# Kernel tuning notes

Measured on AMD Instinct MI355X. Metric: run time of the kernel, lower is better.

## Reference

```python
import jax, jax.numpy as jnp
import numpy as np

B, T, D = 2, 2048, 1024
N, H = 16, 64  # num_heads, head_dim
LOG2E = 1.442695041
NEG_INF = -1.0e9


def setup_inputs() -> dict:
    key = jax.random.key(0)
    ks = jax.random.split(key, 6)
    return {
        "input_tensor": jax.random.normal(ks[0], (B, T, D), dtype=jnp.float32),
        "attention_mask": jax.random.randint(ks[1], (B, 1, T, T), 0, 2, dtype=jnp.int32),
        "wq": jax.random.normal(ks[2], (D, N, H), dtype=jnp.float32),
        "bq": jnp.zeros((N, H), dtype=jnp.float32),
        "wk": jax.random.normal(ks[3], (D, N, H), dtype=jnp.float32),
        "bk": jnp.zeros((N, H), dtype=jnp.float32),
        "wv": jax.random.normal(ks[4], (D, N, H), dtype=jnp.float32),
        "bv": jnp.zeros((N, H), dtype=jnp.float32),
        "wo": jax.random.normal(ks[5], (D, N, H), dtype=jnp.float32),
        "bo": jnp.zeros((D,), dtype=jnp.float32),
        "per_dim_scale": jnp.zeros((H,), dtype=jnp.float32),
    }


def reference(input_tensor, attention_mask, wq, bq, wk, bk, wv, bv, wo, bo, per_dim_scale):
    # QKV projections: [B,T,D] x [D,N,H] -> [B,T,N,H]
    q = jnp.einsum('btd,dnh->btnh', input_tensor, wq) + bq
    k = jnp.einsum('btd,dnh->btnh', input_tensor, wk) + bk
    v = jnp.einsum('btd,dnh->btnh', input_tensor, wv) + bv
    # per-dim query scaling: (log2(e)/sqrt(H)) * softplus(per_dim_scale)
    scale = (LOG2E / jnp.sqrt(jnp.asarray(H, q.dtype))) * jax.nn.softplus(per_dim_scale)
    q = q * scale
    # scores: [B,N,T,S]
    scores = jnp.einsum('btnh,bsnh->bnts', q, k)
    scores = jnp.where(attention_mask == 0, jnp.asarray(NEG_INF, scores.dtype), scores)
    weights = jax.nn.softmax(scores, axis=-1)
    # AV: [B,N,T,S] x [B,S,N,H] -> [B,T,N,H]
    attn_out = jnp.einsum('bnts,bsnh->btnh', weights, v)
    # output projection: [B,T,N,H] x [D,N,H] -> [B,T,D]
    return jnp.einsum('btnh,dnh->btd', attn_out, wo) + bo
```

## Files before the change

kernel.cpp:

```cpp
#include <hip/hip_runtime.h>
#include <math.h>

typedef __bf16 bf16;
typedef __attribute__((ext_vector_type(8))) __bf16 bf16x8;
typedef __attribute__((ext_vector_type(4))) __bf16 bf16x4;
typedef __attribute__((ext_vector_type(4))) float f32x4;

#define BB 2
#define TT 2048
#define DD 1024
#define NHD 16
#define HD 64
#define MM (BB*TT)
#define LOG2E_F 1.442695041f
#define NEGINF_F (-1.0e9f)

__device__ __forceinline__ void gld16(const bf16* g, bf16* l)
{
    __builtin_amdgcn_global_load_lds(
        (const __attribute__((address_space(1))) unsigned int*)g,
        (__attribute__((address_space(3))) unsigned int*)l, 16, 0, 0);
}

__global__ __launch_bounds__(256)
void prep_all(const float* __restrict__ X, const int* __restrict__ m,
              const float* __restrict__ wq, const float* __restrict__ wk,
              const float* __restrict__ wv, const float* __restrict__ wo,
              bf16* __restrict__ Xh, bf16* __restrict__ Xl,
              bf16* __restrict__ qkh, bf16* __restrict__ qkl,
              bf16* __restrict__ vh, bf16* __restrict__ ob,
              unsigned char* __restrict__ bits)
{
    __shared__ float tile[32][33];
    const int bid = blockIdx.x;
    const int t   = threadIdx.x;

    if (bid < 4096) {
        int i = bid * 256 + t;
        float4 v = ((const float4*)X)[i];
        float f[4] = {v.x, v.y, v.z, v.w};
        bf16x4 h, l;
        #pragma unroll
        for (int j = 0; j < 4; ++j) {
            bf16 hh = (bf16)f[j];
            h[j] = hh;
            l[j] = (bf16)(f[j] - (float)hh);
        }
        *(bf16x4*)(Xh + (size_t)i * 4) = h;
        *(bf16x4*)(Xl + (size_t)i * 4) = l;
        return;
    }
    if (bid < 8192) {
        const int idx = bid - 4096;
        const int z   = idx >> 10;
        const int bx  = (idx & 31) << 5;
        const int by  = ((idx >> 5) & 31) << 5;
        const int r   = t >> 3;
        const int c4  = (t & 7) << 2;
        if (z == 3) {
            float4 v = *(const float4*)(wo + (size_t)(by + r) * 1024 + bx + c4);
            bf16x4 o = { (bf16)v.x, (bf16)v.y, (bf16)v.z, (bf16)v.w };
            *(bf16x4*)(ob + (size_t)(by + r) * 1024 + bx + c4) = o;
            return;
        }
        const float* src = (z == 0) ? wq : ((z == 1) ? wk : wv);
        bf16* oh = (z == 0) ? qkh : ((z == 1) ? qkh + 1048576 : vh);
        bf16* ol = (z == 0) ? qkl : ((z == 1) ? qkl + 1048576 : nullptr);
        float4 v = *(const float4*)(src + (size_t)(by + r) * 1024 + bx + c4);
        tile[r][c4+0] = v.x; tile[r][c4+1] = v.y;
        tile[r][c4+2] = v.z; tile[r][c4+3] = v.w;
        __syncthreads();
        bf16x4 hv, lv;
        #pragma unroll
        for (int j = 0; j < 4; ++j) {
            float f = tile[c4 + j][r];
            bf16 h = (bf16)f;
            hv[j] = h;
            lv[j] = (bf16)(f - (float)h);
        }
        *(bf16x4*)(oh + (size_t)(bx + r) * 1024 + by + c4) = hv;
        if (ol)
            *(bf16x4*)(ol + (size_t)(bx + r) * 1024 + by + c4) = lv;
        return;
    }
    {
        int i = (bid - 8192) * 256 + t;
        const int4* mp = (const int4*)m + (size_t)i * 2;
        int4 a  = mp[0];
        int4 b4 = mp[1];
        unsigned v = (a.x  != 0)       | ((a.y  != 0) << 1)
                   | ((a.z  != 0) << 2) | ((a.w  != 0) << 3)
                   | ((b4.x != 0) << 4) | ((b4.y != 0) << 5)
                   | ((b4.z != 0) << 6) | ((b4.w != 0) << 7);
        bits[i] = (unsigned char)v;
    }
}

__global__ __launch_bounds__(256)
void gemm_proj(const bf16* __restrict__ Xh, const bf16* __restrict__ Xl,
               const bf16* __restrict__ Wh, const bf16* __restrict__ Wl,
               const bf16* __restrict__ Wvh,
               const float* __restrict__ bq, const float* __restrict__ bk,
               const float* __restrict__ bv, const float* __restrict__ pds,
               bf16* __restrict__ oQh, bf16* __restrict__ oQl,
               bf16* __restrict__ oKh, bf16* __restrict__ oKl,
               bf16* __restrict__ oVt)
{
    __shared__ bf16 S[4][128 * 32];

    const int bid  = blockIdx.x;
    const int t    = threadIdx.x;
    const int lane = t & 63;
    const int w    = t >> 6;
    const int quad = lane >> 4, l15 = lane & 15;
    const int wm   = (w >> 1) << 6;
    const int wn   = (w & 1)  << 6;

    const int jr0 = ((w * 2 + 0) << 4) + (lane >> 2);
    const int jr1 = ((w * 2 + 1) << 4) + (lane >> 2);
    const int kch = (lane & 3) << 3;
    const int off0 = (w * 2 + 0) * 512;
    const int off1 = (w * 2 + 1) * 512;

    if (bid < 512) {
        const int m0 = (bid >> 4) << 7;
        const int n0 = (bid & 15) << 7;
        bf16* Ah = S[0]; bf16* Al = S[1]; bf16* Bh = S[2]; bf16* Bl = S[3];

        const bf16* pAh0 = Xh + (size_t)(m0 + jr0) * DD + kch;
        const bf16* pAh1 = Xh + (size_t)(m0 + jr1) * DD + kch;
        const bf16* pAl0 = Xl + (size_t)(m0 + jr0) * DD + kch;
        const bf16* pAl1 = Xl + (size_t)(m0 + jr1) * DD + kch;
        const bf16* pBh0 = Wh + (size_t)(n0 + jr0) * DD + kch;
        const bf16* pBh1 = Wh + (size_t)(n0 + jr1) * DD + kch;
        const bf16* pBl0 = Wl + (size_t)(n0 + jr0) * DD + kch;
        const bf16* pBl1 = Wl + (size_t)(n0 + jr1) * DD + kch;

        f32x4 acc[4][4] = {};

        for (int k0 = 0; k0 < DD; k0 += 32) {
            __syncthreads();
            gld16(pAh0 + k0, Ah + off0);  gld16(pAh1 + k0, Ah + off1);
            gld16(pAl0 + k0, Al + off0);  gld16(pAl1 + k0, Al + off1);
            gld16(pBh0 + k0, Bh + off0);  gld16(pBh1 + k0, Bh + off1);
            gld16(pBl0 + k0, Bl + off0);  gld16(pBl1 + k0, Bl + off1);
            __syncthreads();

            bf16x8 ah[4], bh[4];
            #pragma unroll
            for (int mt = 0; mt < 4; ++mt)
                ah[mt] = *(const bf16x8*)(Ah + (wm + (mt << 4) + l15) * 32 + (quad << 3));
            #pragma unroll
            for (int nt = 0; nt < 4; ++nt)
                bh[nt] = *(const bf16x8*)(Bh + (wn + (nt << 4) + l15) * 32 + (quad << 3));
            #pragma unroll
            for (int mt = 0; mt < 4; ++mt)
                #pragma unroll
                for (int nt = 0; nt < 4; ++nt)
                    acc[mt][nt] = __builtin_amdgcn_mfma_f32_16x16x32_bf16(
                        ah[mt], bh[nt], acc[mt][nt], 0, 0, 0);

            bf16x8 bl[4];
            #pragma unroll
            for (int nt = 0; nt < 4; ++nt)
                bl[nt] = *(const bf16x8*)(Bl + (wn + (nt << 4) + l15) * 32 + (quad << 3));
            #pragma unroll
            for (int mt = 0; mt < 4; ++mt)
                #pragma unroll
                for (int nt = 0; nt < 4; ++nt)
                    acc[mt][nt] = __builtin_amdgcn_mfma_f32_16x16x32_bf16(
                        ah[mt], bl[nt], acc[mt][nt], 0, 0, 0);

            bf16x8 al[4];
            #pragma unroll
            for (int mt = 0; mt < 4; ++mt)
                al[mt] = *(const bf16x8*)(Al + (wm + (mt << 4) + l15) * 32 + (quad << 3));
            #pragma unroll
            for (int mt = 0; mt < 4; ++mt)
                #pragma unroll
                for (int nt = 0; nt < 4; ++nt)
                    acc[mt][nt] = __builtin_amdgcn_mfma_f32_16x16x32_bf16(
                        al[mt], bh[nt], acc[mt][nt], 0, 0, 0);
        }

        #pragma unroll
        for (int nt = 0; nt < 4; ++nt) {
            const int col = n0 + wn + (nt << 4) + l15;
            const int isQ = (col < 1024);
            const int nh  = col & 1023;
            const int n   = nh >> 6, h = nh & 63;
            const float bcol = isQ ? bq[nh] : bk[nh];
            float s = 1.f;
            if (isQ) {
                float x  = pds[h];
                float sp = fmaxf(x, 0.f) + log1pf(expf(-fabsf(x)));
                s = (LOG2E_F * LOG2E_F / 8.0f) * sp;
            }
            bf16* dH = isQ ? oQh : oKh;
            bf16* dL = isQ ? oQl : oKl;
            #pragma unroll
            for (int mt = 0; mt < 4; ++mt) {
                #pragma unroll
                for (int reg = 0; reg < 4; ++reg) {
                    const int row = m0 + wm + (mt << 4) + (quad << 2) + reg;
                    const int bi  = row >> 11;
                    const int tt  = row & (TT - 1);
                    float val = (acc[mt][nt][reg] + bcol) * s;
                    const size_t idx = (((size_t)bi * NHD + n) * TT + tt) * HD + h;
                    bf16 hi = (bf16)val;
                    dH[idx] = hi;
                    dL[idx] = (bf16)(val - (float)hi);
                }
            }
        }
    } else {
        const int idx = bid - 512;
        const int m0  = (idx >> 5) << 7;
        const int n0  = (idx & 31) << 7;
        bf16* As = S[0]; bf16* Bs = S[2];

        const bf16* Ap0 = Wvh + (size_t)(m0 + jr0) * DD + kch;
        const bf16* Ap1 = Wvh + (size_t)(m0 + jr1) * DD + kch;
        const bf16* Bp0 = Xh  + (size_t)(n0 + jr0) * DD + kch;
        const bf16* Bp1 = Xh  + (size_t)(n0 + jr1) * DD + kch;

        f32x4 acc[4][4] = {};

        for (int k0 = 0; k0 < DD; k0 += 32) {
            __syncthreads();
            gld16(Ap0 + k0, As + off0);
            gld16(Ap1 + k0, As + off1);
            gld16(Bp0 + k0, Bs + off0);
            gld16(Bp1 + k0, Bs + off1);
            __syncthreads();
            bf16x8 af[4], bfm[4];
            #pragma unroll
            for (int mt = 0; mt < 4; ++mt)
                af[mt] = *(const bf16x8*)(As + (wm + (mt << 4) + l15) * 32 + (quad << 3));
            #pragma unroll
            for (int nt = 0; nt < 4; ++nt)
                bfm[nt] = *(const bf16x8*)(Bs + (wn + (nt << 4) + l15) * 32 + (quad << 3));
            #pragma unroll
            for (int mt = 0; mt < 4; ++mt)
                #pragma unroll
                for (int nt = 0; nt < 4; ++nt)
                    acc[mt][nt] = __builtin_amdgcn_mfma_f32_16x16x32_bf16(
                        af[mt], bfm[nt], acc[mt][nt], 0, 0, 0);
        }

        #pragma unroll
        for (int nt = 0; nt < 4; ++nt) {
            const int col = n0 + wn + (nt << 4) + l15;
            const int bi  = col >> 11;
            const int tt  = col & (TT - 1);
            #pragma unroll
            for (int mt = 0; mt < 4; ++mt) {
                #pragma unroll
                for (int reg = 0; reg < 4; ++reg) {
                    const int row = m0 + wm + (mt << 4) + (quad << 2) + reg;
                    float val = acc[mt][nt][reg] + bv[row];
                    oVt[((size_t)bi * 1024 + row) * TT + tt] = (bf16)val;
                }
            }
        }
    }
}

__global__ __launch_bounds__(256)
void gemm_out(const bf16* __restrict__ A, const bf16* __restrict__ Bt,
              const float* __restrict__ bias, float* __restrict__ oF)
{
    __shared__ bf16 As[128 * 32];
    __shared__ bf16 Bs[64 * 32];

    const int t    = threadIdx.x;
    const int lane = t & 63;
    const int w    = t >> 6;
    const int quad = lane >> 4, l15 = lane & 15;
    const int m0   = blockIdx.y << 7;
    const int n0   = blockIdx.x << 6;
    const int wm   = (w >> 1) << 6;
    const int wn   = (w & 1)  << 5;

    const int jr0 = ((w * 2 + 0) << 4) + (lane >> 2);
    const int jr1 = ((w * 2 + 1) << 4) + (lane >> 2);
    const int jrB = (w << 4) + (lane >> 2);
    const int kch = (lane & 3) << 3;

    bf16* lA0 = As + (w * 2 + 0) * 512;
    bf16* lA1 = As + (w * 2 + 1) * 512;
    bf16* lB  = Bs + w * 512;

    const bf16* Ap0 = A  + (size_t)(m0 + jr0) * DD + kch;
    const bf16* Ap1 = A  + (size_t)(m0 + jr1) * DD + kch;
    const bf16* Bp  = Bt + (size_t)(n0 + jrB) * DD + kch;

    f32x4 acc[4][2] = {};

    for (int k0 = 0; k0 < DD; k0 += 32) {
        __syncthreads();
        gld16(Ap0 + k0, lA0);
        gld16(Ap1 + k0, lA1);
        gld16(Bp + k0, lB);
        __syncthreads();
        bf16x8 af[4], bfm[2];
        #pragma unroll
        for (int mt = 0; mt < 4; ++mt)
            af[mt] = *(const bf16x8*)(As + (wm + (mt << 4) + l15) * 32 + (quad << 3));
        #pragma unroll
        for (int nt = 0; nt < 2; ++nt)
            bfm[nt] = *(const bf16x8*)(Bs + (wn + (nt << 4) + l15) * 32 + (quad << 3));
        #pragma unroll
        for (int mt = 0; mt < 4; ++mt)
            #pragma unroll
            for (int nt = 0; nt < 2; ++nt)
                acc[mt][nt] = __builtin_amdgcn_mfma_f32_16x16x32_bf16(
                    af[mt], bfm[nt], acc[mt][nt], 0, 0, 0);
    }

    #pragma unroll
    for (int nt = 0; nt < 2; ++nt) {
        const int col = n0 + wn + (nt << 4) + l15;
        const float bcol = bias[col];
        #pragma unroll
        for (int mt = 0; mt < 4; ++mt) {
            #pragma unroll
            for (int reg = 0; reg < 4; ++reg) {
                const int row = m0 + wm + (mt << 4) + (quad << 2) + reg;
                oF[(size_t)row * DD + col] = acc[mt][nt][reg] + bcol;
            }
        }
    }
}

__global__ __launch_bounds__(512)
void attn_mfma(const bf16* __restrict__ Qh, const bf16* __restrict__ Ql,
               const bf16* __restrict__ Kh, const bf16* __restrict__ Kl,
               const bf16* __restrict__ Vt,
               const unsigned long long* __restrict__ mb64,
               bf16* __restrict__ AO)
{
    __shared__ bf16 Ksh[64][64];
    __shared__ bf16 Ksl[64][64];
    __shared__ bf16 Vts[64][64];
    __shared__ bf16 Ps[8][16][64];
    __shared__ unsigned long long msk64[128];

    const int t    = threadIdx.x;
    const int lane = t & 63;
    const int w    = t >> 6;
    const int quad = lane >> 4, l15 = lane & 15;
    const int bn   = blockIdx.y;
    const int b    = bn >> 4, n = bn & 15;
    const int q0   = blockIdx.x << 7;

    const bf16* Qbh = Qh + (size_t)bn * TT * HD;
    const bf16* Qbl = Ql + (size_t)bn * TT * HD;
    const bf16* Kbh = Kh + (size_t)bn * TT * HD;
    const bf16* Kbl = Kl + (size_t)bn * TT * HD;
    const bf16* Vtb = Vt + (size_t)bn * HD * TT;

    const int qrow = q0 + (w << 4) + l15;
    bf16x8 qfh[2], qfl[2];
    qfh[0] = *(const bf16x8*)(Qbh + (size_t)qrow * HD + (quad << 3));
    qfh[1] = *(const bf16x8*)(Qbh + (size_t)qrow * HD + 32 + (quad << 3));
    qfl[0] = *(const bf16x8*)(Qbl + (size_t)qrow * HD + (quad << 3));
    qfl[1] = *(const bf16x8*)(Qbl + (size_t)qrow * HD + 32 + (quad << 3));

    f32x4 O[4];
    #pragma unroll
    for (int i = 0; i < 4; ++i) O[i] = (f32x4){0.f,0.f,0.f,0.f};
    float m_i = -INFINITY;
    float l_i = 0.f;

    const int rS = t >> 3;
    const int cG = (t & 7) << 3;
    const int cL = (((t & 7) ^ (rS & 7)) << 3);
    const int sw8 = (l15 & 7) << 3;

    for (int kb = 0; kb < TT; kb += 64) {
        bf16x8 khv = *(const bf16x8*)(Kbh + (size_t)(kb + rS) * HD + cG);
        bf16x8 klv = *(const bf16x8*)(Kbl + (size_t)(kb + rS) * HD + cG);
        bf16x8 vv  = *(const bf16x8*)(Vtb + (size_t)rS * TT + kb + cG);
        unsigned long long mw = 0;
        if (t < 128)
            mw = mb64[((size_t)b * TT + q0 + t) * (TT / 64) + (kb >> 6)];

        __syncthreads();
        *(bf16x8*)&Ksh[rS][cL] = khv;
        *(bf16x8*)&Ksl[rS][cL] = klv;
        *(bf16x8*)&Vts[rS][cL] = vv;
        if (t < 128) msk64[t] = mw;
        __syncthreads();

        f32x4 s_acc[4];
        #pragma unroll
        for (int i = 0; i < 4; ++i) s_acc[i] = (f32x4){0.f,0.f,0.f,0.f};
        __builtin_amdgcn_s_setprio(1);
        #pragma unroll
        for (int k2 = 0; k2 < 2; ++k2) {
            #pragma unroll
            for (int nt = 0; nt < 4; ++nt) {
                bf16x8 bkh = *(const bf16x8*)&Ksh[(nt << 4) + l15][((k2 << 5) + (quad << 3)) ^ sw8];
                bf16x8 bkl = *(const bf16x8*)&Ksl[(nt << 4) + l15][((k2 << 5) + (quad << 3)) ^ sw8];
                s_acc[nt] = __builtin_amdgcn_mfma_f32_16x16x32_bf16(bkh, qfh[k2], s_acc[nt], 0, 0, 0);
                s_acc[nt] = __builtin_amdgcn_mfma_f32_16x16x32_bf16(bkl, qfh[k2], s_acc[nt], 0, 0, 0);
                s_acc[nt] = __builtin_amdgcn_mfma_f32_16x16x32_bf16(bkh, qfl[k2], s_acc[nt], 0, 0, 0);
            }
        }
        __builtin_amdgcn_s_setprio(0);

        const unsigned long long word = msk64[(w << 4) + l15];
        const unsigned w0 = (unsigned)word;
        const unsigned w1 = (unsigned)(word >> 32);
        float sv[16];
        #pragma unroll
        for (int nt = 0; nt < 4; ++nt) {
            const unsigned wrd = (nt & 2) ? w1 : w0;
            #pragma unroll
            for (int reg = 0; reg < 4; ++reg) {
                const int bit = ((nt & 1) << 4) + (quad << 2) + reg;
                sv[nt * 4 + reg] = ((wrd >> bit) & 1u) ? s_acc[nt][reg] : NEGINF_F;
            }
        }
        float a0 = fmaxf(sv[0], sv[1]),  a1 = fmaxf(sv[2], sv[3]);
        float a2 = fmaxf(sv[4], sv[5]),  a3 = fmaxf(sv[6], sv[7]);
        float a4 = fmaxf(sv[8], sv[9]),  a5 = fmaxf(sv[10], sv[11]);
        float a6 = fmaxf(sv[12], sv[13]), a7 = fmaxf(sv[14], sv[15]);
        float b0 = fmaxf(a0, a1), b1 = fmaxf(a2, a3);
        float b2 = fmaxf(a4, a5), b3 = fmaxf(a6, a7);
        float mx = fmaxf(fmaxf(b0, b1), fmaxf(b2, b3));
        mx = fmaxf(mx, __shfl_xor(mx, 16));
        mx = fmaxf(mx, __shfl_xor(mx, 32));

        if (!__all(mx <= m_i + 8.0f)) {
            const float mnew  = fmaxf(m_i, mx);
            const float alpha = exp2f(m_i - mnew);
            l_i *= alpha;
            #pragma unroll
            for (int nt = 0; nt < 4; ++nt) {
                O[nt][0] *= alpha; O[nt][1] *= alpha;
                O[nt][2] *= alpha; O[nt][3] *= alpha;
            }
            m_i = mnew;
        }

        float p[16];
        #pragma unroll
        for (int i = 0; i < 16; ++i) p[i] = exp2f(sv[i] - m_i);
        float s0 = (p[0] + p[1]) + (p[2] + p[3]);
        float s1 = (p[4] + p[5]) + (p[6] + p[7]);
        float s2 = (p[8] + p[9]) + (p[10] + p[11]);
        float s3 = (p[12] + p[13]) + (p[14] + p[15]);
        float sum = (s0 + s1) + (s2 + s3);
        sum += __shfl_xor(sum, 16);
        sum += __shfl_xor(sum, 32);
        l_i += sum;

        #pragma unroll
        for (int nt = 0; nt < 4; ++nt) {
            bf16x4 pv = { (bf16)p[nt * 4 + 0], (bf16)p[nt * 4 + 1],
                          (bf16)p[nt * 4 + 2], (bf16)p[nt * 4 + 3] };
            *(bf16x4*)&Ps[w][l15][((nt << 4) + (quad << 2)) ^ sw8] = pv;
        }

        __builtin_amdgcn_s_setprio(1);
        #pragma unroll
        for (int s2i = 0; s2i < 2; ++s2i) {
            bf16x8 ap = *(const bf16x8*)&Ps[w][l15][((s2i << 5) + (quad << 3)) ^ sw8];
            #pragma unroll
            for (int nt = 0; nt < 4; ++nt) {
                bf16x8 bv = *(const bf16x8*)&Vts[(nt << 4) + l15][((s2i << 5) + (quad << 3)) ^ sw8];
                O[nt] = __builtin_amdgcn_mfma_f32_16x16x32_bf16(bv, ap, O[nt], 0, 0, 0);
            }
        }
        __builtin_amdgcn_s_setprio(0);
    }

    {
        const float inv = 1.0f / l_i;
        const size_t base = ((size_t)b * TT + qrow) * (NHD * HD) + (size_t)n * HD;
        #pragma unroll
        for (int nt = 0; nt < 4; ++nt) {
            bf16x4 o = { (bf16)(O[nt][0] * inv), (bf16)(O[nt][1] * inv),
                         (bf16)(O[nt][2] * inv), (bf16)(O[nt][3] * inv) };
            *(bf16x4*)(AO + base + (nt << 4) + (quad << 2)) = o;
        }
    }
}

extern "C" void kernel_launch(void* const* d_in, const int* in_sizes, int n_in,
                              void* d_out, int out_size, void* d_ws, size_t ws_size,
                              hipStream_t stream)
{
    const float* X   = (const float*)d_in[0];
    const int*   msk = (const int*)d_in[1];
    const float* wq  = (const float*)d_in[2];
    const float* bq  = (const float*)d_in[3];
    const float* wk  = (const float*)d_in[4];
    const float* bk  = (const float*)d_in[5];
    const float* wv  = (const float*)d_in[6];
    const float* bv  = (const float*)d_in[7];
    const float* wo  = (const float*)d_in[8];
    const float* bo  = (const float*)d_in[9];
    const float* pds = (const float*)d_in[10];
    float* out = (float*)d_out;

    bf16* ws   = (bf16*)d_ws;
    bf16* Xh   = ws;
    bf16* Xl   = ws + 4194304;
    bf16* WQKh = ws + 8388608;
    bf16* WQKl = ws + 10485760;
    bf16* Wvh  = ws + 12582912;
    bf16* Wob  = ws + 13631488;
    bf16* Qhb  = ws + 14680064;
    bf16* Qlb  = ws + 18874368;
    bf16* Khb  = ws + 23068672;
    bf16* Klb  = ws + 27262976;
    unsigned char* mbits = (unsigned char*)(ws + 31457280);
    bf16* Vtb  = ws + 32505856;
    bf16* AOb  = Xh;

    dim3 blk(256);

    prep_all<<<12288, blk, 0, stream>>>(X, msk, wq, wk, wv, wo,
                                        Xh, Xl, WQKh, WQKl, Wvh, Wob, mbits);

    gemm_proj<<<768, blk, 0, stream>>>(
        Xh, Xl, WQKh, WQKl, Wvh, bq, bk, bv, pds,
        Qhb, Qlb, Khb, Klb, Vtb);

    dim3 ga(TT / 128, BB * NHD);
    attn_mfma<<<ga, dim3(512), 0, stream>>>(
        Qhb, Qlb, Khb, Klb, Vtb, (const unsigned long long*)mbits, AOb);

    gemm_out<<<dim3(16, 32), blk, 0, stream>>>(AOb, Wob, bo, out);
}
```

Baseline: 312.9 us.

## Split attention KV range across two warp groups with in-block softmax merge

```diff
diff --git a/kernel.cpp b/kernel.cpp
--- a/kernel.cpp
+++ b/kernel.cpp
@@ -333,26 +333,26 @@
     }
 }
 
-__global__ __launch_bounds__(512)
+__global__ __launch_bounds__(512, 6)
 void attn_mfma(const bf16* __restrict__ Qh, const bf16* __restrict__ Ql,
                const bf16* __restrict__ Kh, const bf16* __restrict__ Kl,
                const bf16* __restrict__ Vt,
                const unsigned long long* __restrict__ mb64,
                bf16* __restrict__ AO)
 {
-    __shared__ bf16 Ksh[64][64];
-    __shared__ bf16 Ksl[64][64];
-    __shared__ bf16 Vts[64][64];
-    __shared__ bf16 Ps[8][16][64];
-    __shared__ unsigned long long msk64[128];
+    __shared__ bf16 KH[2][64 * 64];
+    __shared__ bf16 KL[2][64 * 64];
+    __shared__ bf16 PS[8][16 * 64];
+    __shared__ unsigned long long MSK[2][64];
 
     const int t    = threadIdx.x;
     const int lane = t & 63;
     const int w    = t >> 6;
+    const int g    = w >> 2;
     const int quad = lane >> 4, l15 = lane & 15;
     const int bn   = blockIdx.y;
     const int b    = bn >> 4, n = bn & 15;
-    const int q0   = blockIdx.x << 7;
+    const int q0   = blockIdx.x << 6;
 
     const bf16* Qbh = Qh + (size_t)bn * TT * HD;
     const bf16* Qbl = Ql + (size_t)bn * TT * HD;
@@ -360,7 +360,7 @@
     const bf16* Kbl = Kl + (size_t)bn * TT * HD;
     const bf16* Vtb = Vt + (size_t)bn * HD * TT;
 
-    const int qrow = q0 + (w << 4) + l15;
+    const int qrow = q0 + ((w & 3) << 4) + l15;
     bf16x8 qfh[2], qfl[2];
     qfh[0] = *(const bf16x8*)(Qbh + (size_t)qrow * HD + (quad << 3));
     qfh[1] = *(const bf16x8*)(Qbh + (size_t)qrow * HD + 32 + (quad << 3));
@@ -373,24 +373,37 @@
     float m_i = -INFINITY;
     float l_i = 0.f;
 
-    const int rS = t >> 3;
-    const int cG = (t & 7) << 3;
-    const int cL = (((t & 7) ^ (rS & 7)) << 3);
+    const int tg  = t & 255;
+    const int rS  = tg >> 2;
+    const int cp  = tg & 3;
+    const int cG0 = (cp * 2    ) << 3;
+    const int cG1 = (cp * 2 + 1) << 3;
+    const int cL0 = (((cp * 2    ) ^ (rS & 7))) << 3;
+    const int cL1 = (((cp * 2 + 1) ^ (rS & 7))) << 3;
     const int sw8 = (l15 & 7) << 3;
 
-    for (int kb = 0; kb < TT; kb += 64) {
-        bf16x8 khv = *(const bf16x8*)(Kbh + (size_t)(kb + rS) * HD + cG);
-        bf16x8 klv = *(const bf16x8*)(Kbl + (size_t)(kb + rS) * HD + cG);
-        bf16x8 vv  = *(const bf16x8*)(Vtb + (size_t)rS * TT + kb + cG);
+    for (int it = 0; it < 16; ++it) {
+        const int kb = (g << 10) + (it << 6);
+        const bf16* kr = Kbh + (size_t)(kb + rS) * HD;
+        const bf16* lr = Kbl + (size_t)(kb + rS) * HD;
+        const bf16* vr = Vtb + (size_t)rS * TT + kb;
+        bf16x8 kh0 = *(const bf16x8*)(kr + cG0);
+        bf16x8 kh1 = *(const bf16x8*)(kr + cG1);
+        bf16x8 kl0 = *(const bf16x8*)(lr + cG0);
+        bf16x8 kl1 = *(const bf16x8*)(lr + cG1);
+        bf16x8 v0  = *(const bf16x8*)(vr + cG0);
+        bf16x8 v1  = *(const bf16x8*)(vr + cG1);
         unsigned long long mw = 0;
         if (t < 128)
-            mw = mb64[((size_t)b * TT + q0 + t) * (TT / 64) + (kb >> 6)];
-
-        __syncthreads();
-        *(bf16x8*)&Ksh[rS][cL] = khv;
-        *(bf16x8*)&Ksl[rS][cL] = klv;
-        *(bf16x8*)&Vts[rS][cL] = vv;
-        if (t < 128) msk64[t] = mw;
+            mw = mb64[((size_t)b * TT + q0 + (t & 63)) * (TT / 64)
+                      + ((t >> 6) << 4) + it];
+
+        __syncthreads();
+        *(bf16x8*)&KH[g][rS * 64 + cL0] = kh0;
+        *(bf16x8*)&KH[g][rS * 64 + cL1] = kh1;
+        *(bf16x8*)&KL[g][rS * 64 + cL0] = kl0;
+        *(bf16x8*)&KL[g][rS * 64 + cL1] = kl1;
+        if (t < 128) MSK[t >> 6][t & 63] = mw;
         __syncthreads();
 
         f32x4 s_acc[4];
@@ -401,8 +414,10 @@
         for (int k2 = 0; k2 < 2; ++k2) {
             #pragma unroll
             for (int nt = 0; nt < 4; ++nt) {
-                bf16x8 bkh = *(const bf16x8*)&Ksh[(nt << 4) + l15][((k2 << 5) + (quad << 3)) ^ sw8];
-                bf16x8 bkl = *(const bf16x8*)&Ksl[(nt << 4) + l15][((k2 << 5) + (quad << 3)) ^ sw8];
+                const int ro = ((nt << 4) + l15) * 64;
+                const int co = ((k2 << 5) + (quad << 3)) ^ sw8;
+                bf16x8 bkh = *(const bf16x8*)&KH[g][ro + co];
+                bf16x8 bkl = *(const bf16x8*)&KL[g][ro + co];
                 s_acc[nt] = __builtin_amdgcn_mfma_f32_16x16x32_bf16(bkh, qfh[k2], s_acc[nt], 0, 0, 0);
                 s_acc[nt] = __builtin_amdgcn_mfma_f32_16x16x32_bf16(bkl, qfh[k2], s_acc[nt], 0, 0, 0);
                 s_acc[nt] = __builtin_amdgcn_mfma_f32_16x16x32_bf16(bkh, qfl[k2], s_acc[nt], 0, 0, 0);
@@ -410,7 +425,7 @@
         }
         __builtin_amdgcn_s_setprio(0);
 
-        const unsigned long long word = msk64[(w << 4) + l15];
+        const unsigned long long word = MSK[g][((w & 3) << 4) + l15];
         const unsigned w0 = (unsigned)word;
         const unsigned w1 = (unsigned)(word >> 32);
         float sv[16];
@@ -461,30 +476,65 @@
         for (int nt = 0; nt < 4; ++nt) {
             bf16x4 pv = { (bf16)p[nt * 4 + 0], (bf16)p[nt * 4 + 1],
                           (bf16)p[nt * 4 + 2], (bf16)p[nt * 4 + 3] };
-            *(bf16x4*)&Ps[w][l15][((nt << 4) + (quad << 2)) ^ sw8] = pv;
-        }
+            *(bf16x4*)&PS[w][l15 * 64 + (((nt << 4) + (quad << 2)) ^ sw8)] = pv;
+        }
+
+        __syncthreads();
+        *(bf16x8*)&KL[g][rS * 64 + cL0] = v0;
+        *(bf16x8*)&KL[g][rS * 64 + cL1] = v1;
+        __syncthreads();
 
         __builtin_amdgcn_s_setprio(1);
         #pragma unroll
         for (int s2i = 0; s2i < 2; ++s2i) {
-            bf16x8 ap = *(const bf16x8*)&Ps[w][l15][((s2i << 5) + (quad << 3)) ^ sw8];
+            bf16x8 ap = *(const bf16x8*)&PS[w][l15 * 64 + (((s2i << 5) + (quad << 3)) ^ sw8)];
             #pragma unroll
             for (int nt = 0; nt < 4; ++nt) {
-                bf16x8 bv = *(const bf16x8*)&Vts[(nt << 4) + l15][((s2i << 5) + (quad << 3)) ^ sw8];
+                bf16x8 bv = *(const bf16x8*)&KL[g][((nt << 4) + l15) * 64
+                                                   + (((s2i << 5) + (quad << 3)) ^ sw8)];
                 O[nt] = __builtin_amdgcn_mfma_f32_16x16x32_bf16(bv, ap, O[nt], 0, 0, 0);
             }
         }
         __builtin_amdgcn_s_setprio(0);
     }
 
-    {
-        const float inv = 1.0f / l_i;
-        const size_t base = ((size_t)b * TT + qrow) * (NHD * HD) + (size_t)n * HD;
+    float* OMp = (float*)&KH[0][0];
+    float* MLp = (float*)&KL[0][0];
+    __syncthreads();
+    if (w >= 4) {
+        const int base = (w - 4) << 10;
+        #pragma unroll
+        for (int nt = 0; nt < 4; ++nt)
+            #pragma unroll
+            for (int reg = 0; reg < 4; ++reg) {
+                const int h = (nt << 4) + (quad << 2) + reg;
+                OMp[base + h * 16 + l15] = O[nt][reg];
+            }
+        if (quad == 0) {
+            MLp[((w - 4) << 5) + (l15 << 1)    ] = m_i;
+            MLp[((w - 4) << 5) + (l15 << 1) + 1] = l_i;
+        }
+    }
+    __syncthreads();
+    if (w < 4) {
+        const float m1v = MLp[(w << 5) + (l15 << 1)];
+        const float l1v = MLp[(w << 5) + (l15 << 1) + 1];
+        const float mm  = fmaxf(m_i, m1v);
+        const float f0  = exp2f(m_i - mm);
+        const float f1  = exp2f(m1v - mm);
+        const float inv = 1.0f / (l_i * f0 + l1v * f1);
+        const int   ob  = w << 10;
+        const size_t basew = ((size_t)b * TT + qrow) * (NHD * HD) + (size_t)n * HD;
         #pragma unroll
         for (int nt = 0; nt < 4; ++nt) {
-            bf16x4 o = { (bf16)(O[nt][0] * inv), (bf16)(O[nt][1] * inv),
-                         (bf16)(O[nt][2] * inv), (bf16)(O[nt][3] * inv) };
-            *(bf16x4*)(AO + base + (nt << 4) + (quad << 2)) = o;
+            bf16x4 o;
+            #pragma unroll
+            for (int reg = 0; reg < 4; ++reg) {
+                const int h = (nt << 4) + (quad << 2) + reg;
+                const float o1 = OMp[ob + h * 16 + l15];
+                o[reg] = (bf16)((O[nt][reg] * f0 + o1 * f1) * inv);
+            }
+            *(bf16x4*)(AO + basew + (nt << 4) + (quad << 2)) = o;
         }
     }
 }
@@ -530,7 +580,7 @@
         Xh, Xl, WQKh, WQKl, Wvh, bq, bk, bv, pds,
         Qhb, Qlb, Khb, Klb, Vtb);
 
-    dim3 ga(TT / 128, BB * NHD);
+    dim3 ga(TT / 64, BB * NHD);
     attn_mfma<<<ga, dim3(512), 0, stream>>>(
         Qhb, Qlb, Khb, Klb, Vtb, (const unsigned long long*)mbits, AOb);
 
```

Result: slower. 499.3 us (+59.6%).

## Shrink attention blocks to 256 threads and alias V onto K-low LDS

Applied to the files above, without the earlier changes.

```diff
diff --git a/kernel.cpp b/kernel.cpp
--- a/kernel.cpp
+++ b/kernel.cpp
@@ -333,18 +333,17 @@
     }
 }
 
-__global__ __launch_bounds__(512)
+__global__ __launch_bounds__(256, 5)
 void attn_mfma(const bf16* __restrict__ Qh, const bf16* __restrict__ Ql,
                const bf16* __restrict__ Kh, const bf16* __restrict__ Kl,
                const bf16* __restrict__ Vt,
                const unsigned long long* __restrict__ mb64,
                bf16* __restrict__ AO)
 {
-    __shared__ bf16 Ksh[64][64];
-    __shared__ bf16 Ksl[64][64];
-    __shared__ bf16 Vts[64][64];
-    __shared__ bf16 Ps[8][16][64];
-    __shared__ unsigned long long msk64[128];
+    __shared__ bf16 KH[64 * 64];
+    __shared__ bf16 KLV[64 * 64];
+    __shared__ bf16 PS[4][16 * 64];
+    __shared__ unsigned long long MSK[64];
 
     const int t    = threadIdx.x;
     const int lane = t & 63;
@@ -352,7 +351,7 @@
     const int quad = lane >> 4, l15 = lane & 15;
     const int bn   = blockIdx.y;
     const int b    = bn >> 4, n = bn & 15;
-    const int q0   = blockIdx.x << 7;
+    const int q0   = blockIdx.x << 6;
 
     const bf16* Qbh = Qh + (size_t)bn * TT * HD;
     const bf16* Qbl = Ql + (size_t)bn * TT * HD;
@@ -373,25 +372,37 @@
     float m_i = -INFINITY;
     float l_i = 0.f;
 
-    const int rS = t >> 3;
-    const int cG = (t & 7) << 3;
-    const int cL = (((t & 7) ^ (rS & 7)) << 3);
+    const int rS  = t >> 2;
+    const int cp  = t & 3;
+    const int cG0 = (cp * 2    ) << 3;
+    const int cG1 = (cp * 2 + 1) << 3;
+    const int cL0 = ((cp * 2    ) ^ (rS & 7)) << 3;
+    const int cL1 = ((cp * 2 + 1) ^ (rS & 7)) << 3;
     const int sw8 = (l15 & 7) << 3;
 
-    for (int kb = 0; kb < TT; kb += 64) {
-        bf16x8 khv = *(const bf16x8*)(Kbh + (size_t)(kb + rS) * HD + cG);
-        bf16x8 klv = *(const bf16x8*)(Kbl + (size_t)(kb + rS) * HD + cG);
-        bf16x8 vv  = *(const bf16x8*)(Vtb + (size_t)rS * TT + kb + cG);
+    for (int it = 0; it < 32; ++it) {
+        const int kb = it << 6;
+        const bf16* kr = Kbh + (size_t)(kb + rS) * HD;
+        const bf16* lr = Kbl + (size_t)(kb + rS) * HD;
+        bf16x8 kh0 = *(const bf16x8*)(kr + cG0);
+        bf16x8 kh1 = *(const bf16x8*)(kr + cG1);
+        bf16x8 kl0 = *(const bf16x8*)(lr + cG0);
+        bf16x8 kl1 = *(const bf16x8*)(lr + cG1);
         unsigned long long mw = 0;
-        if (t < 128)
-            mw = mb64[((size_t)b * TT + q0 + t) * (TT / 64) + (kb >> 6)];
-
-        __syncthreads();
-        *(bf16x8*)&Ksh[rS][cL] = khv;
-        *(bf16x8*)&Ksl[rS][cL] = klv;
-        *(bf16x8*)&Vts[rS][cL] = vv;
-        if (t < 128) msk64[t] = mw;
-        __syncthreads();
+        if (t < 64)
+            mw = mb64[((size_t)b * TT + q0 + t) * (TT / 64) + it];
+
+        __syncthreads();
+        *(bf16x8*)&KH [rS * 64 + cL0] = kh0;
+        *(bf16x8*)&KH [rS * 64 + cL1] = kh1;
+        *(bf16x8*)&KLV[rS * 64 + cL0] = kl0;
+        *(bf16x8*)&KLV[rS * 64 + cL1] = kl1;
+        if (t < 64) MSK[t] = mw;
+        __syncthreads();
+
+        const bf16* vr = Vtb + (size_t)rS * TT + kb;
+        bf16x8 v0 = *(const bf16x8*)(vr + cG0);
+        bf16x8 v1 = *(const bf16x8*)(vr + cG1);
 
         f32x4 s_acc[4];
         #pragma unroll
@@ -401,8 +412,10 @@
         for (int k2 = 0; k2 < 2; ++k2) {
             #pragma unroll
             for (int nt = 0; nt < 4; ++nt) {
-                bf16x8 bkh = *(const bf16x8*)&Ksh[(nt << 4) + l15][((k2 << 5) + (quad << 3)) ^ sw8];
-                bf16x8 bkl = *(const bf16x8*)&Ksl[(nt << 4) + l15][((k2 << 5) + (quad << 3)) ^ sw8];
+                const int ro = ((nt << 4) + l15) * 64;
+                const int co = ((k2 << 5) + (quad << 3)) ^ sw8;
+                bf16x8 bkh = *(const bf16x8*)&KH [ro + co];
+                bf16x8 bkl = *(const bf16x8*)&KLV[ro + co];
                 s_acc[nt] = __builtin_amdgcn_mfma_f32_16x16x32_bf16(bkh, qfh[k2], s_acc[nt], 0, 0, 0);
                 s_acc[nt] = __builtin_amdgcn_mfma_f32_16x16x32_bf16(bkl, qfh[k2], s_acc[nt], 0, 0, 0);
                 s_acc[nt] = __builtin_amdgcn_mfma_f32_16x16x32_bf16(bkh, qfl[k2], s_acc[nt], 0, 0, 0);
@@ -410,7 +423,7 @@
         }
         __builtin_amdgcn_s_setprio(0);
 
-        const unsigned long long word = msk64[(w << 4) + l15];
+        const unsigned long long word = MSK[(w << 4) + l15];
         const unsigned w0 = (unsigned)word;
         const unsigned w1 = (unsigned)(word >> 32);
         float sv[16];
@@ -461,16 +474,22 @@
         for (int nt = 0; nt < 4; ++nt) {
             bf16x4 pv = { (bf16)p[nt * 4 + 0], (bf16)p[nt * 4 + 1],
                           (bf16)p[nt * 4 + 2], (bf16)p[nt * 4 + 3] };
-            *(bf16x4*)&Ps[w][l15][((nt << 4) + (quad << 2)) ^ sw8] = pv;
-        }
+            *(bf16x4*)&PS[w][l15 * 64 + (((nt << 4) + (quad << 2)) ^ sw8)] = pv;
+        }
+
+        __syncthreads();
+        *(bf16x8*)&KLV[rS * 64 + cL0] = v0;
+        *(bf16x8*)&KLV[rS * 64 + cL1] = v1;
+        __syncthreads();
 
         __builtin_amdgcn_s_setprio(1);
         #pragma unroll
         for (int s2i = 0; s2i < 2; ++s2i) {
-            bf16x8 ap = *(const bf16x8*)&Ps[w][l15][((s2i << 5) + (quad << 3)) ^ sw8];
+            bf16x8 ap = *(const bf16x8*)&PS[w][l15 * 64 + (((s2i << 5) + (quad << 3)) ^ sw8)];
             #pragma unroll
             for (int nt = 0; nt < 4; ++nt) {
-                bf16x8 bv = *(const bf16x8*)&Vts[(nt << 4) + l15][((s2i << 5) + (quad << 3)) ^ sw8];
+                bf16x8 bv = *(const bf16x8*)&KLV[((nt << 4) + l15) * 64
+                                                 + (((s2i << 5) + (quad << 3)) ^ sw8)];
                 O[nt] = __builtin_amdgcn_mfma_f32_16x16x32_bf16(bv, ap, O[nt], 0, 0, 0);
             }
         }
@@ -530,8 +549,8 @@
         Xh, Xl, WQKh, WQKl, Wvh, bq, bk, bv, pds,
         Qhb, Qlb, Khb, Klb, Vtb);
 
-    dim3 ga(TT / 128, BB * NHD);
-    attn_mfma<<<ga, dim3(512), 0, stream>>>(
+    dim3 ga(TT / 64, BB * NHD);
+    attn_mfma<<<ga, dim3(256), 0, stream>>>(
         Qhb, Qlb, Khb, Klb, Vtb, (const unsigned long long*)mbits, AOb);
 
     gemm_out<<<dim3(16, 32), blk, 0, stream>>>(AOb, Wob, bo, out);
```

Measured after the change: 386.4 us. 23.5% more time.
